# Optimization experiments

Measured on AMD Instinct MI355X. Metric: run time of the kernel, lower is better.

Reference implementation:

```python
import jax, jax.numpy as jnp
import numpy as np

HEADS = 4
DIM_HEAD = 32
IN_CHANNELS = 256
SCALE = DIM_HEAD ** -0.5
EPS = 1e-5


def setup_inputs() -> dict:
    key = jax.random.key(0)
    ks = jax.random.split(key, 6)
    B, C, H, W = 16, IN_CHANNELS, 64, 64
    inner = HEADS * DIM_HEAD  # 128
    x = jax.random.normal(ks[0], (B, C, H, W), dtype=jnp.float32)
    # 1x1 conv weights are [out_ch, in_ch] (kernel spatial dims are 1)
    w_qkv = jax.random.normal(ks[1], (3 * inner, C), dtype=jnp.float32) * (C ** -0.5)
    w_out = jax.random.normal(ks[2], (C, inner), dtype=jnp.float32) * (inner ** -0.5)
    b_out = jax.random.normal(ks[3], (C,), dtype=jnp.float32) * 0.01
    gn_gamma = jnp.ones((C,), dtype=jnp.float32)
    gn_beta = jnp.zeros((C,), dtype=jnp.float32)
    return {"x": x, "w_qkv": w_qkv, "w_out": w_out, "b_out": b_out,
            "gn_gamma": gn_gamma, "gn_beta": gn_beta}


def reference(x, w_qkv, w_out, b_out, gn_gamma, gn_beta):
    b, c, h, w = x.shape
    n = h * w
    inner = HEADS * DIM_HEAD
    # 1x1 conv (no bias): [b, 3*inner, h, w], then chunk into q,k,v along channels
    qkv = jnp.einsum('oc,bchw->bohw', w_qkv, x)
    qkv = qkv.reshape(b, 3, HEADS, DIM_HEAD, n)  # chunk + 'b (h c) x y -> b h c (x y)'
    q, k, v = qkv[:, 0], qkv[:, 1], qkv[:, 2]    # each [b, heads, dim_head, n]
    q = jax.nn.softmax(q, axis=-2) * SCALE       # softmax over dim_head axis
    k = jax.nn.softmax(k, axis=-1)               # softmax over spatial axis
    context = jnp.einsum('bhdn,bhen->bhde', k, v)  # [b, heads, d, e]
    out = jnp.einsum('bhde,bhdn->bhen', context, q)  # [b, heads, e, n]
    out = out.reshape(b, inner, h, w)            # 'b h c (x y) -> b (h c) x y'
    # out 1x1 conv with bias
    out = jnp.einsum('oc,bchw->bohw', w_out, out) + b_out[None, :, None, None]
    # GroupNorm(num_groups=1): normalize over (C,H,W) per sample, per-channel affine
    mean = jnp.mean(out, axis=(1, 2, 3), keepdims=True)
    var = jnp.var(out, axis=(1, 2, 3), keepdims=True)
    out = (out - mean) * jax.lax.rsqrt(var + EPS)
    return out * gn_gamma[None, :, None, None] + gn_beta[None, :, None, None]
```

## Files before the change

kernel.cpp:

```cpp
#include <hip/hip_runtime.h>
#include <hip/hip_bf16.h>
#include <math.h>

#define B_SZ 16
#define C_IN 256
#define HEADS 4
#define DHEAD 32
#define INNER 128
#define QKV_CH 384
#define N_PIX 4096
#define SCALE_Q 0.17677669529663687f
#define GN_EPS 1e-5f
#define NCHK 32

typedef __attribute__((ext_vector_type(8))) short s16x8;
typedef __attribute__((ext_vector_type(4))) float f32x4;
typedef __attribute__((ext_vector_type(8))) unsigned short u16x8;
typedef __attribute__((ext_vector_type(4))) unsigned short u16x4;

__device__ __forceinline__ float waveSum(float v) {
#pragma unroll
  for (int off = 32; off > 0; off >>= 1) v += __shfl_down(v, off, 64);
  return v;
}
__device__ __forceinline__ unsigned short f2bf(float f) {
  unsigned int u = __builtin_bit_cast(unsigned int, f);
  unsigned int r = 0x7FFFu + ((u >> 16) & 1u);
  return (unsigned short)((u + r) >> 16);
}
__device__ __forceinline__ float bf2f(unsigned short u) {
  unsigned int x = ((unsigned int)u) << 16;
  return __builtin_bit_cast(float, x);
}

__global__ __launch_bounds__(256) void cvt_w(const float* __restrict__ wq,
                                             const float* __restrict__ wo,
                                             unsigned short* __restrict__ wqb,
                                             unsigned short* __restrict__ wob) {
  const int i = blockIdx.x * 256 + threadIdx.x;
  if (i < QKV_CH * C_IN) wqb[i] = f2bf(wq[i]);
  if (i < C_IN * INNER) wob[i] = f2bf(wo[i]);
}

__global__ __launch_bounds__(512, 4) void qkv_gemm(const unsigned short* __restrict__ A,
                                                   const float* __restrict__ X,
                                                   unsigned short* __restrict__ Out) {
  const int b = blockIdx.y;
  const int n0 = blockIdx.x * 64;
  const int tid = threadIdx.x;
  const int w = tid >> 6, l = tid & 63;
  const int lr = l & 15, kg = l >> 4;
  const int wm = w >> 1, wn = w & 1;

  __shared__ char lds[65536];
  char* As = lds;
  char* Bs = lds + 49152;

  const float* xb = X + (size_t)b * C_IN * N_PIX;
  const int c_loc = ((tid >> 3) & 7) + w * 8;
  const int oct = tid & 7;

  auto ISSUE_A = [&](int kc, int half) {
#pragma unroll
    for (int it = 0; it < 3; ++it) {
      const int idx = it * 512 + tid;
      const int r = idx >> 3;
      const int srcb = ((idx & 7) << 4) ^ ((r & 7) << 4);
      __builtin_amdgcn_global_load_lds(
          (const __attribute__((address_space(1))) void*)((const char*)A +
              ((size_t)(half * 192 + r) * C_IN + kc * 64) * 2 + srcb),
          (__attribute__((address_space(3))) void*)(As + half * 24576 + idx * 16), 16, 0, 0);
    }
  };

  f32x4 xr0, xr1;
  auto ISSUE_X = [&](int kc) {
    const float* xp = xb + (size_t)(kc * 64 + c_loc) * N_PIX + n0 + oct * 8;
    xr0 = *reinterpret_cast<const f32x4*>(xp);
    xr1 = *reinterpret_cast<const f32x4*>(xp + 4);
  };

  auto WRITE_B = [&](int pb) {
#pragma unroll
    for (int j = 0; j < 8; ++j) {
      const int n = oct * 8 + j;
      const float v = (j < 4) ? xr0[j] : xr1[j - 4];
      *reinterpret_cast<unsigned short*>(
          Bs + pb * 8192 + n * 128 + ((2 * c_loc) ^ (((n ^ (n >> 3)) & 7) << 4))) = f2bf(v);
    }
  };

  f32x4 acc[2][3][2] = {};

  auto COMPUTE = [&](int kc, int half) {
    const char* Ab = As + half * 24576;
    const char* Bb = Bs + (kc & 1) * 8192;
#pragma unroll
    for (int ks = 0; ks < 2; ++ks) {
      const int kb = ks * 64 + kg * 16;
      s16x8 av[3], bv[2];
#pragma unroll
      for (int i = 0; i < 3; ++i) {
        const int r = wm * 48 + i * 16 + lr;
        av[i] = *reinterpret_cast<const s16x8*>(Ab + r * 128 + (kb ^ ((r & 7) << 4)));
      }
#pragma unroll
      for (int j = 0; j < 2; ++j) {
        const int n = wn * 32 + j * 16 + lr;
        bv[j] = *reinterpret_cast<const s16x8*>(Bb + n * 128 +
                                                (kb ^ (((n ^ (n >> 3)) & 7) << 4)));
      }
#pragma unroll
      for (int i = 0; i < 3; ++i)
#pragma unroll
        for (int j = 0; j < 2; ++j)
          acc[half][i][j] =
              __builtin_amdgcn_mfma_f32_16x16x32_bf16(av[i], bv[j], acc[half][i][j], 0, 0, 0);
    }
  };

  ISSUE_A(0, 0);
  ISSUE_X(0);
  asm volatile("s_waitcnt vmcnt(0)" ::: "memory");
  WRITE_B(0);
  asm volatile("s_waitcnt lgkmcnt(0)" ::: "memory");
  __builtin_amdgcn_s_barrier();

  for (int kc = 0; kc < 4; ++kc) {
    ISSUE_A(kc, 1);
    if (kc < 3) {
      ISSUE_X(kc + 1);
      asm volatile("s_waitcnt vmcnt(5)" ::: "memory");
    } else {
      asm volatile("s_waitcnt vmcnt(3)" ::: "memory");
    }
    __builtin_amdgcn_s_barrier();
    COMPUTE(kc, 0);
    asm volatile("s_waitcnt lgkmcnt(0)" ::: "memory");
    __builtin_amdgcn_s_barrier();
    if (kc < 3) {
      ISSUE_A(kc + 1, 0);
      asm volatile("s_waitcnt vmcnt(3)" ::: "memory");
    } else {
      asm volatile("s_waitcnt vmcnt(0)" ::: "memory");
    }
    __builtin_amdgcn_s_barrier();
    if (kc < 3) WRITE_B((kc + 1) & 1);
    COMPUTE(kc, 1);
    asm volatile("s_waitcnt lgkmcnt(0)" ::: "memory");
    __builtin_amdgcn_s_barrier();
  }

  unsigned short* Ob = Out + (size_t)b * QKV_CH * N_PIX;
#pragma unroll
  for (int half = 0; half < 2; ++half)
#pragma unroll
    for (int i = 0; i < 3; ++i) {
      const int mrow = half * 192 + wm * 48 + i * 16 + kg * 4;
#pragma unroll
      for (int j = 0; j < 2; ++j) {
        const int col = n0 + wn * 32 + j * 16 + lr;
#pragma unroll
        for (int r = 0; r < 4; ++r)
          Ob[(size_t)(mrow + r) * N_PIX + col] = f2bf(acc[half][i][j][r]);
      }
    }
}

__global__ __launch_bounds__(256) void ctx_mfma(const unsigned short* __restrict__ qkv,
                                                float* __restrict__ ctxp,
                                                float* __restrict__ mpart,
                                                float* __restrict__ spart) {
  const int wid = blockIdx.x * 4 + (threadIdx.x >> 6);
  const int l = threadIdx.x & 63;
  const int b = wid >> 7;
  const int h = (wid >> 5) & 3;
  const int c = wid & 31;
  const int lr = l & 15, kg = l >> 4;
  const unsigned short* kb =
      qkv + ((size_t)b * QKV_CH + INNER + h * DHEAD) * N_PIX + c * 128 + kg * 8;
  const unsigned short* vb = kb + (size_t)INNER * N_PIX;

  u16x8 kf[2][4], vf[2][4];
#pragma unroll
  for (int dt = 0; dt < 2; ++dt)
#pragma unroll
    for (int ks = 0; ks < 4; ++ks) {
      kf[dt][ks] = *reinterpret_cast<const u16x8*>(kb + (size_t)(dt * 16 + lr) * N_PIX + ks * 32);
      vf[dt][ks] = *reinterpret_cast<const u16x8*>(vb + (size_t)(dt * 16 + lr) * N_PIX + ks * 32);
    }
  float kv[2][4][8];
  float m[2] = {-INFINITY, -INFINITY};
#pragma unroll
  for (int dt = 0; dt < 2; ++dt)
#pragma unroll
    for (int ks = 0; ks < 4; ++ks)
#pragma unroll
      for (int j = 0; j < 8; ++j) {
        kv[dt][ks][j] = bf2f(kf[dt][ks][j]);
        m[dt] = fmaxf(m[dt], kv[dt][ks][j]);
      }
#pragma unroll
  for (int dt = 0; dt < 2; ++dt) {
    m[dt] = fmaxf(m[dt], __shfl_xor(m[dt], 16, 64));
    m[dt] = fmaxf(m[dt], __shfl_xor(m[dt], 32, 64));
  }
  float s[2] = {0.f, 0.f};
  s16x8 ka[2][4];
#pragma unroll
  for (int dt = 0; dt < 2; ++dt)
#pragma unroll
    for (int ks = 0; ks < 4; ++ks)
#pragma unroll
      for (int j = 0; j < 8; ++j) {
        const float e = __expf(kv[dt][ks][j] - m[dt]);
        s[dt] += e;
        ka[dt][ks][j] = (short)f2bf(e);
      }
#pragma unroll
  for (int dt = 0; dt < 2; ++dt) {
    s[dt] += __shfl_xor(s[dt], 16, 64);
    s[dt] += __shfl_xor(s[dt], 32, 64);
  }
  f32x4 acc[2][2] = {};
#pragma unroll
  for (int ks = 0; ks < 4; ++ks)
#pragma unroll
    for (int dt = 0; dt < 2; ++dt)
#pragma unroll
      for (int et = 0; et < 2; ++et)
        acc[dt][et] = __builtin_amdgcn_mfma_f32_16x16x32_bf16(
            ka[dt][ks], __builtin_bit_cast(s16x8, vf[et][ks]), acc[dt][et], 0, 0, 0);

  float* cp = ctxp + (size_t)wid * 1024;
#pragma unroll
  for (int dt = 0; dt < 2; ++dt)
#pragma unroll
    for (int et = 0; et < 2; ++et)
#pragma unroll
      for (int r = 0; r < 4; ++r)
        cp[(dt * 16 + kg * 4 + r) * 32 + et * 16 + lr] = acc[dt][et][r];
  if (kg == 0) {
    mpart[wid * 32 + lr] = m[0];
    mpart[wid * 32 + 16 + lr] = m[1];
    spart[wid * 32 + lr] = s[0];
    spart[wid * 32 + 16 + lr] = s[1];
  }
}

__global__ __launch_bounds__(256) void ctx_reduce(const float* __restrict__ ctxp,
                                                  const float* __restrict__ mpart,
                                                  const float* __restrict__ spart,
                                                  float* __restrict__ ctxf) {
  const int bh = blockIdx.x;
  const int tid = threadIdx.x;
  __shared__ float ms[NCHK][32], ss[NCHK][32], fac[NCHK][32];
  __shared__ float inv_l[32];
#pragma unroll
  for (int i = 0; i < 4; ++i) {
    const int idx = tid + i * 256;
    ms[idx >> 5][idx & 31] = mpart[(size_t)bh * 1024 + idx];
    ss[idx >> 5][idx & 31] = spart[(size_t)bh * 1024 + idx];
  }
  __syncthreads();
  if (tid < 32) {
    const int d = tid;
    float M = -INFINITY;
    for (int c = 0; c < NCHK; ++c) M = fmaxf(M, ms[c][d]);
    float den = 0.f;
    for (int c = 0; c < NCHK; ++c) {
      const float f = __expf(ms[c][d] - M);
      fac[c][d] = f;
      den += f * ss[c][d];
    }
    inv_l[d] = 1.0f / den;
  }
  __syncthreads();
  const float* cp = ctxp + (size_t)bh * (NCHK * 1024);
#pragma unroll
  for (int i = 0; i < 4; ++i) {
    const int idx = tid + i * 256;
    const int d = idx >> 5;
    float a = 0.f;
    for (int c = 0; c < NCHK; ++c) a += fac[c][d] * cp[(size_t)c * 1024 + idx];
    ctxf[(size_t)bh * 1024 + idx] = a * inv_l[d];
  }
}

__global__ __launch_bounds__(256) void weff_k(const unsigned short* __restrict__ wo,
                                              const float* __restrict__ ctxf,
                                              unsigned short* __restrict__ weff) {
  const int b = blockIdx.z, h = blockIdx.y, oq = blockIdx.x;
  const int tid = threadIdx.x;
  const int o = oq * 64 + (tid >> 2);
  const int d0 = (tid & 3) * 8;

  float wr[32];
  const unsigned short* wp = wo + (size_t)o * INNER + h * DHEAD;
#pragma unroll
  for (int e8 = 0; e8 < 4; ++e8) {
    u16x8 v = *reinterpret_cast<const u16x8*>(wp + e8 * 8);
#pragma unroll
    for (int j = 0; j < 8; ++j) wr[e8 * 8 + j] = bf2f(v[j]);
  }
  const float* cb = ctxf + (size_t)(b * HEADS + h) * 1024;
  u16x8 outv;
#pragma unroll
  for (int dd = 0; dd < 8; ++dd) {
    const float* cr = cb + (size_t)(d0 + dd) * 32;
    float acc = 0.f;
#pragma unroll
    for (int e4 = 0; e4 < 8; ++e4) {
      const f32x4 c4 = *reinterpret_cast<const f32x4*>(cr + e4 * 4);
#pragma unroll
      for (int j = 0; j < 4; ++j) acc += wr[e4 * 4 + j] * c4[j];
    }
    outv[dd] = f2bf(acc);
  }
  unsigned short* op = weff + ((size_t)b * C_IN + o) * INNER + h * DHEAD + d0;
  *reinterpret_cast<u16x8*>(op) = outv;
}

__global__ __launch_bounds__(256) void q_softmax(const unsigned short* __restrict__ qkv,
                                                 unsigned short* __restrict__ qsm_t) {
  const int b = blockIdx.z, h = blockIdx.y;
  const int n = blockIdx.x * 256 + threadIdx.x;
  const unsigned short* qb = qkv + ((size_t)b * QKV_CH + h * DHEAD) * N_PIX + n;
  float q[32];
  float m = -INFINITY;
#pragma unroll
  for (int d2 = 0; d2 < 32; ++d2) {
    q[d2] = bf2f(qb[(size_t)d2 * N_PIX]);
    m = fmaxf(m, q[d2]);
  }
  float s = 0.f;
#pragma unroll
  for (int d2 = 0; d2 < 32; ++d2) {
    q[d2] = __expf(q[d2] - m);
    s += q[d2];
  }
  const float inv = SCALE_Q / s;
  unsigned short* ob = qsm_t + ((size_t)b * N_PIX + n) * INNER + h * DHEAD;
#pragma unroll
  for (int d8 = 0; d8 < 4; ++d8) {
    u16x8 pk;
#pragma unroll
    for (int r = 0; r < 8; ++r) pk[r] = f2bf(q[d8 * 8 + r] * inv);
    *reinterpret_cast<u16x8*>(&ob[d8 * 8]) = pk;
  }
}

template <bool WRITE>
__global__ __launch_bounds__(256) void out_gemm_t(
    const unsigned short* __restrict__ A, const unsigned short* __restrict__ Bm,
    float* __restrict__ Out, const float* __restrict__ bias,
    float* __restrict__ gn_part, const float* __restrict__ gamma,
    const float* __restrict__ beta) {
  const int b = blockIdx.z;
  const int m0 = blockIdx.y * 128;
  const int n0 = blockIdx.x * 128;
  const int tid = threadIdx.x;
  const int w = tid >> 6, l = tid & 63;
  const int lr = l & 15, kg = l >> 4;
  const int mOff = (w >> 1) * 64, nOff = (w & 1) * 64;

  __shared__ unsigned short As[8192];
  __shared__ unsigned short Bs[8192];
  __shared__ float red[8];

  const unsigned short* Ab = A + (size_t)b * C_IN * INNER;
  const unsigned short* Bb = Bm + (size_t)b * N_PIX * INNER;
  f32x4 acc[4][4] = {};

  for (int kc = 0; kc < INNER; kc += 64) {
#pragma unroll
    for (int s = 0; s < 4; ++s) {
      const int blk = (w * 4 + s) * 64 + l;
      const int r = blk >> 3;
      const int c = ((blk & 7) ^ (r & 7)) << 3;
      __builtin_amdgcn_global_load_lds(
          (const __attribute__((address_space(1))) void*)(Ab + (size_t)(m0 + r) * INNER + kc + c),
          (__attribute__((address_space(3))) void*)((char*)As + (w * 4 + s) * 1024), 16, 0, 0);
      __builtin_amdgcn_global_load_lds(
          (const __attribute__((address_space(1))) void*)(Bb + (size_t)(n0 + r) * INNER + kc + c),
          (__attribute__((address_space(3))) void*)((char*)Bs + (w * 4 + s) * 1024), 16, 0, 0);
    }
    __syncthreads();
#pragma unroll
    for (int ks = 0; ks < 2; ++ks) {
      const int kbyte = ks * 64 + kg * 16;
      s16x8 av[4], bv[4];
#pragma unroll
      for (int i = 0; i < 4; ++i) {
        const int row = mOff + i * 16 + lr;
        av[i] = *reinterpret_cast<const s16x8*>(
            (const char*)As + row * 128 + (kbyte ^ ((row & 7) << 4)));
      }
#pragma unroll
      for (int j = 0; j < 4; ++j) {
        const int row = nOff + j * 16 + lr;
        bv[j] = *reinterpret_cast<const s16x8*>(
            (const char*)Bs + row * 128 + (kbyte ^ ((row & 7) << 4)));
      }
#pragma unroll
      for (int i = 0; i < 4; ++i)
#pragma unroll
        for (int j = 0; j < 4; ++j)
          acc[i][j] = __builtin_amdgcn_mfma_f32_16x16x32_bf16(av[i], bv[j], acc[i][j], 0, 0, 0);
    }
    __syncthreads();
  }

  if (!WRITE) {
    float s = 0.f, s2 = 0.f;
#pragma unroll
    for (int i = 0; i < 4; ++i) {
      const int rowb = m0 + mOff + i * 16 + kg * 4;
#pragma unroll
      for (int r = 0; r < 4; ++r) {
        const float bvs = bias[rowb + r];
#pragma unroll
        for (int j = 0; j < 4; ++j) {
          const float v = acc[i][j][r] + bvs;
          s += v;
          s2 += v * v;
        }
      }
    }
    const float S = waveSum(s), S2 = waveSum(s2);
    if (l == 0) {
      red[w] = S;
      red[4 + w] = S2;
    }
    __syncthreads();
    if (tid == 0) {
      const int bid = (b * 2 + blockIdx.y) * 32 + blockIdx.x;
      gn_part[(size_t)bid * 2 + 0] = red[0] + red[1] + red[2] + red[3];
      gn_part[(size_t)bid * 2 + 1] = red[4] + red[5] + red[6] + red[7];
    }
  } else {
    const int i64 = tid & 63;
    float ps = gn_part[(size_t)(b * 64 + i64) * 2 + 0];
    float ps2 = gn_part[(size_t)(b * 64 + i64) * 2 + 1];
    ps = waveSum(ps);
    ps2 = waveSum(ps2);
    const float invn = 1.0f / (float)(C_IN * N_PIX);
    const float mean = __shfl(ps, 0, 64) * invn;
    const float var = __shfl(ps2, 0, 64) * invn - mean * mean;
    const float istd = rsqrtf(var + GN_EPS);

    float* Ob = Out + (size_t)b * C_IN * N_PIX;
#pragma unroll
    for (int i = 0; i < 4; ++i) {
      const int rowb = m0 + mOff + i * 16 + kg * 4;
#pragma unroll
      for (int r = 0; r < 4; ++r) {
        const int ch = rowb + r;
        const float bvs = bias[ch];
        const float g = gamma[ch] * istd;
        const float be = beta[ch];
#pragma unroll
        for (int j = 0; j < 4; ++j) {
          const int col = n0 + nOff + j * 16 + lr;
          const float v = acc[i][j][r] + bvs;
          Ob[(size_t)ch * N_PIX + col] = (v - mean) * g + be;
        }
      }
    }
  }
}

extern "C" void kernel_launch(void* const* d_in, const int* in_sizes, int n_in,
                              void* d_out, int out_size, void* d_ws, size_t ws_size,
                              hipStream_t stream) {
  const float* x = (const float*)d_in[0];
  const float* w_qkv = (const float*)d_in[1];
  const float* w_out = (const float*)d_in[2];
  const float* b_out = (const float*)d_in[3];
  const float* gamma = (const float*)d_in[4];
  const float* beta = (const float*)d_in[5];
  float* out = (float*)d_out;

  char* p = (char*)d_ws;
  unsigned short* qkv_bf = (unsigned short*)p; p += (size_t)B_SZ * QKV_CH * N_PIX * 2;
  unsigned short* qsm_t = (unsigned short*)p;  p += (size_t)B_SZ * N_PIX * INNER * 2;
  unsigned short* wq_bf = (unsigned short*)p;  p += (size_t)QKV_CH * C_IN * 2;
  unsigned short* wo_bf = (unsigned short*)p;  p += (size_t)C_IN * INNER * 2;
  float* ctxp = (float*)p;    p += (size_t)B_SZ * HEADS * NCHK * 1024 * 4;
  float* mpart = (float*)p;   p += (size_t)B_SZ * HEADS * NCHK * 32 * 4;
  float* spart = (float*)p;   p += (size_t)B_SZ * HEADS * NCHK * 32 * 4;
  float* ctxf = (float*)p;    p += (size_t)B_SZ * HEADS * 1024 * 4;
  unsigned short* weff = (unsigned short*)p; p += (size_t)B_SZ * C_IN * INNER * 2;
  float* gn_part = (float*)p; p += (size_t)1024 * 2 * 4;

  cvt_w<<<dim3(384), 256, 0, stream>>>(w_qkv, w_out, wq_bf, wo_bf);
  qkv_gemm<<<dim3(64, B_SZ), 512, 0, stream>>>(wq_bf, x, qkv_bf);
  ctx_mfma<<<dim3(512), 256, 0, stream>>>(qkv_bf, ctxp, mpart, spart);
  ctx_reduce<<<dim3(64), 256, 0, stream>>>(ctxp, mpart, spart, ctxf);
  weff_k<<<dim3(4, HEADS, B_SZ), 256, 0, stream>>>(wo_bf, ctxf, weff);
  q_softmax<<<dim3(16, HEADS, B_SZ), 256, 0, stream>>>(qkv_bf, qsm_t);
  out_gemm_t<false><<<dim3(32, 2, B_SZ), 256, 0, stream>>>(
      weff, qsm_t, nullptr, b_out, gn_part, nullptr, nullptr);
  out_gemm_t<true><<<dim3(32, 2, B_SZ), 256, 0, stream>>>(
      weff, qsm_t, out, b_out, gn_part, gamma, beta);
}
```

Measured before the change: 98.91 us.

## Swizzle block order for XCD locality and deepen qkv GEMM load pipeline

Flattens grids and remaps block IDs so consecutive ranks on each of the 8 XCDs cover contiguous batch/pixel ranges. This is meant to improve L2 locality in qkv_gemm, ctx_mfma, q_softmax and out_gemm. qkv_gemm is rewritten as a fully unrolled pipeline: each wave loads only its own A rows, X is double-registered (XA/XB) and prefetched two stages ahead, and vmcnt waits are relaxed with fewer barriers. The risks are more registers per thread and fragile hand-tuned waitcnt ordering.

```diff
diff --git a/kernel.cpp b/kernel.cpp
--- a/kernel.cpp
+++ b/kernel.cpp
@@ -18,6 +18,10 @@
 typedef __attribute__((ext_vector_type(8))) unsigned short u16x8;
 typedef __attribute__((ext_vector_type(4))) unsigned short u16x4;
 
+#define VMCNT(n) asm volatile("s_waitcnt vmcnt(" #n ")" ::: "memory")
+#define LGKMCNT0 asm volatile("s_waitcnt lgkmcnt(0)" ::: "memory")
+#define CFENCE asm volatile("" ::: "memory")
+
 __device__ __forceinline__ float waveSum(float v) {
 #pragma unroll
   for (int off = 32; off > 0; off >>= 1) v += __shfl_down(v, off, 64);
@@ -45,8 +49,10 @@
 __global__ __launch_bounds__(512, 4) void qkv_gemm(const unsigned short* __restrict__ A,
                                                    const float* __restrict__ X,
                                                    unsigned short* __restrict__ Out) {
-  const int b = blockIdx.y;
-  const int n0 = blockIdx.x * 64;
+  const int id = blockIdx.x;
+  const int rank = (id & 7) * 128 + (id >> 3);
+  const int b = rank >> 6;
+  const int n0 = (rank & 63) * 64;
   const int tid = threadIdx.x;
   const int w = tid >> 6, l = tid & 63;
   const int lr = l & 15, kg = l >> 4;
@@ -56,35 +62,49 @@
   char* As = lds;
   char* Bs = lds + 49152;
 
-  const float* xb = X + (size_t)b * C_IN * N_PIX;
   const int c_loc = ((tid >> 3) & 7) + w * 8;
   const int oct = tid & 7;
+  const float* xbase = X + (size_t)b * C_IN * N_PIX + (size_t)c_loc * N_PIX + n0 + oct * 8;
 
   auto ISSUE_A = [&](int kc, int half) {
 #pragma unroll
-    for (int it = 0; it < 3; ++it) {
-      const int idx = it * 512 + tid;
-      const int r = idx >> 3;
-      const int srcb = ((idx & 7) << 4) ^ ((r & 7) << 4);
+    for (int it = 0; it < 6; ++it) {
+      const int idx = it * 64 + l;
+      const int row = wm * 48 + (idx >> 3);
+      const int srcb = ((idx & 7) << 4) ^ ((row & 7) << 4);
       __builtin_amdgcn_global_load_lds(
           (const __attribute__((address_space(1))) void*)((const char*)A +
-              ((size_t)(half * 192 + r) * C_IN + kc * 64) * 2 + srcb),
-          (__attribute__((address_space(3))) void*)(As + half * 24576 + idx * 16), 16, 0, 0);
+              ((size_t)(half * 192 + row) * C_IN + kc * 64) * 2 + srcb),
+          (__attribute__((address_space(3))) void*)(As + half * 24576 + wm * 6144 + idx * 16),
+          16, 0, 0);
     }
   };
 
-  f32x4 xr0, xr1;
-  auto ISSUE_X = [&](int kc) {
-    const float* xp = xb + (size_t)(kc * 64 + c_loc) * N_PIX + n0 + oct * 8;
-    xr0 = *reinterpret_cast<const f32x4*>(xp);
-    xr1 = *reinterpret_cast<const f32x4*>(xp + 4);
+  f32x4 xa0, xa1, xb0, xb1;
+  auto ISSUE_XA = [&](int kc) {
+    const float* xp = xbase + (size_t)(kc * 64) * N_PIX;
+    xa0 = *reinterpret_cast<const f32x4*>(xp);
+    xa1 = *reinterpret_cast<const f32x4*>(xp + 4);
   };
-
-  auto WRITE_B = [&](int pb) {
+  auto ISSUE_XB = [&](int kc) {
+    const float* xp = xbase + (size_t)(kc * 64) * N_PIX;
+    xb0 = *reinterpret_cast<const f32x4*>(xp);
+    xb1 = *reinterpret_cast<const f32x4*>(xp + 4);
+  };
+  auto WRITE_BA = [&](int pb) {
 #pragma unroll
     for (int j = 0; j < 8; ++j) {
       const int n = oct * 8 + j;
-      const float v = (j < 4) ? xr0[j] : xr1[j - 4];
+      const float v = (j < 4) ? xa0[j] : xa1[j - 4];
+      *reinterpret_cast<unsigned short*>(
+          Bs + pb * 8192 + n * 128 + ((2 * c_loc) ^ (((n ^ (n >> 3)) & 7) << 4))) = f2bf(v);
+    }
+  };
+  auto WRITE_BB = [&](int pb) {
+#pragma unroll
+    for (int j = 0; j < 8; ++j) {
+      const int n = oct * 8 + j;
+      const float v = (j < 4) ? xb0[j] : xb1[j - 4];
       *reinterpret_cast<unsigned short*>(
           Bs + pb * 8192 + n * 128 + ((2 * c_loc) ^ (((n ^ (n >> 3)) & 7) << 4))) = f2bf(v);
     }
@@ -119,37 +139,53 @@
     }
   };
 
-  ISSUE_A(0, 0);
-  ISSUE_X(0);
-  asm volatile("s_waitcnt vmcnt(0)" ::: "memory");
-  WRITE_B(0);
-  asm volatile("s_waitcnt lgkmcnt(0)" ::: "memory");
-  __builtin_amdgcn_s_barrier();
-
-  for (int kc = 0; kc < 4; ++kc) {
-    ISSUE_A(kc, 1);
-    if (kc < 3) {
-      ISSUE_X(kc + 1);
-      asm volatile("s_waitcnt vmcnt(5)" ::: "memory");
-    } else {
-      asm volatile("s_waitcnt vmcnt(3)" ::: "memory");
-    }
-    __builtin_amdgcn_s_barrier();
-    COMPUTE(kc, 0);
-    asm volatile("s_waitcnt lgkmcnt(0)" ::: "memory");
-    __builtin_amdgcn_s_barrier();
-    if (kc < 3) {
-      ISSUE_A(kc + 1, 0);
-      asm volatile("s_waitcnt vmcnt(3)" ::: "memory");
-    } else {
-      asm volatile("s_waitcnt vmcnt(0)" ::: "memory");
-    }
-    __builtin_amdgcn_s_barrier();
-    if (kc < 3) WRITE_B((kc + 1) & 1);
-    COMPUTE(kc, 1);
-    asm volatile("s_waitcnt lgkmcnt(0)" ::: "memory");
-    __builtin_amdgcn_s_barrier();
-  }
+  ISSUE_A(0, 0); CFENCE;
+  ISSUE_XA(0);
+  VMCNT(0);
+  WRITE_BA(0);
+  LGKMCNT0;
+  __builtin_amdgcn_s_barrier();
+
+  ISSUE_A(0, 1); CFENCE;
+  ISSUE_XB(1);
+  COMPUTE(0, 0);
+  LGKMCNT0;
+  __builtin_amdgcn_s_barrier();
+  ISSUE_A(1, 0); CFENCE;
+  ISSUE_XA(2);
+  VMCNT(8);
+  WRITE_BB(1);
+  COMPUTE(0, 1);
+  LGKMCNT0;
+  __builtin_amdgcn_s_barrier();
+  ISSUE_A(1, 1);
+  VMCNT(8);
+  COMPUTE(1, 0);
+  LGKMCNT0;
+  __builtin_amdgcn_s_barrier();
+  ISSUE_A(2, 0); CFENCE;
+  ISSUE_XB(3);
+  VMCNT(8);
+  WRITE_BA(0);
+  COMPUTE(1, 1);
+  LGKMCNT0;
+  __builtin_amdgcn_s_barrier();
+  ISSUE_A(2, 1);
+  VMCNT(8);
+  COMPUTE(2, 0);
+  LGKMCNT0;
+  __builtin_amdgcn_s_barrier();
+  ISSUE_A(3, 0);
+  VMCNT(6);
+  WRITE_BB(1);
+  COMPUTE(2, 1);
+  LGKMCNT0;
+  __builtin_amdgcn_s_barrier();
+  ISSUE_A(3, 1);
+  VMCNT(6);
+  COMPUTE(3, 0);
+  VMCNT(0);
+  COMPUTE(3, 1);
 
   unsigned short* Ob = Out + (size_t)b * QKV_CH * N_PIX;
 #pragma unroll
@@ -171,7 +207,9 @@
                                                 float* __restrict__ ctxp,
                                                 float* __restrict__ mpart,
                                                 float* __restrict__ spart) {
-  const int wid = blockIdx.x * 4 + (threadIdx.x >> 6);
+  const int id = blockIdx.x;
+  const int rank = (id & 7) * 64 + (id >> 3);
+  const int wid = rank * 4 + (threadIdx.x >> 6);
   const int l = threadIdx.x & 63;
   const int b = wid >> 7;
   const int h = (wid >> 5) & 3;
@@ -323,8 +361,11 @@
 
 __global__ __launch_bounds__(256) void q_softmax(const unsigned short* __restrict__ qkv,
                                                  unsigned short* __restrict__ qsm_t) {
-  const int b = blockIdx.z, h = blockIdx.y;
-  const int n = blockIdx.x * 256 + threadIdx.x;
+  const int id = blockIdx.x;
+  const int rank = (id & 7) * 128 + (id >> 3);
+  const int b = rank >> 6;
+  const int h = (rank >> 4) & 3;
+  const int n = (rank & 15) * 256 + threadIdx.x;
   const unsigned short* qb = qkv + ((size_t)b * QKV_CH + h * DHEAD) * N_PIX + n;
   float q[32];
   float m = -INFINITY;
@@ -356,9 +397,11 @@
     float* __restrict__ Out, const float* __restrict__ bias,
     float* __restrict__ gn_part, const float* __restrict__ gamma,
     const float* __restrict__ beta) {
-  const int b = blockIdx.z;
-  const int m0 = blockIdx.y * 128;
-  const int n0 = blockIdx.x * 128;
+  const int id = blockIdx.x;
+  const int rank = (id & 7) * 128 + (id >> 3);
+  const int b = rank >> 6;
+  const int m0 = ((rank >> 5) & 1) * 128;
+  const int n0 = (rank & 31) * 128;
   const int tid = threadIdx.x;
   const int w = tid >> 6, l = tid & 63;
   const int lr = l & 15, kg = l >> 4;
@@ -434,9 +477,8 @@
     }
     __syncthreads();
     if (tid == 0) {
-      const int bid = (b * 2 + blockIdx.y) * 32 + blockIdx.x;
-      gn_part[(size_t)bid * 2 + 0] = red[0] + red[1] + red[2] + red[3];
-      gn_part[(size_t)bid * 2 + 1] = red[4] + red[5] + red[6] + red[7];
+      gn_part[(size_t)rank * 2 + 0] = red[0] + red[1] + red[2] + red[3];
+      gn_part[(size_t)rank * 2 + 1] = red[4] + red[5] + red[6] + red[7];
     }
   } else {
     const int i64 = tid & 63;
@@ -494,13 +536,13 @@
   float* gn_part = (float*)p; p += (size_t)1024 * 2 * 4;
 
   cvt_w<<<dim3(384), 256, 0, stream>>>(w_qkv, w_out, wq_bf, wo_bf);
-  qkv_gemm<<<dim3(64, B_SZ), 512, 0, stream>>>(wq_bf, x, qkv_bf);
+  qkv_gemm<<<dim3(1024), 512, 0, stream>>>(wq_bf, x, qkv_bf);
   ctx_mfma<<<dim3(512), 256, 0, stream>>>(qkv_bf, ctxp, mpart, spart);
   ctx_reduce<<<dim3(64), 256, 0, stream>>>(ctxp, mpart, spart, ctxf);
   weff_k<<<dim3(4, HEADS, B_SZ), 256, 0, stream>>>(wo_bf, ctxf, weff);
-  q_softmax<<<dim3(16, HEADS, B_SZ), 256, 0, stream>>>(qkv_bf, qsm_t);
-  out_gemm_t<false><<<dim3(32, 2, B_SZ), 256, 0, stream>>>(
+  q_softmax<<<dim3(1024), 256, 0, stream>>>(qkv_bf, qsm_t);
+  out_gemm_t<false><<<dim3(1024), 256, 0, stream>>>(
       weff, qsm_t, nullptr, b_out, gn_part, nullptr, nullptr);
-  out_gemm_t<true><<<dim3(32, 2, B_SZ), 256, 0, stream>>>(
+  out_gemm_t<true><<<dim3(1024), 256, 0, stream>>>(
       weff, qsm_t, out, b_out, gn_part, gamma, beta);
 }
```

Result: slower. 101.4 us (+2.5%).

## Fuse query softmax into QKV GEMM epilogue and remap blocks for XCD locality

Applied to the files above, without the earlier changes.

The q-channel softmax over the head dimension now runs inside the QKV GEMM epilogue: q accumulators are staged in LDS, softmaxed per pixel and head, and written transposed as bf16. The q channels are no longer stored to the intermediate qkv buffer, and the separate q_softmax kernel is removed. This removes a kernel launch and a full re-read of q from global memory. Separately, the qkv_gemm, ctx_mfma and out_gemm kernels use a 1D grid with a rank permutation ((id&7)*K + id>>3) so that neighbouring tiles land on the same XCD for L2 reuse. In exchange the GEMM epilogue gains an LDS pass and an extra barrier.

```diff
diff --git a/kernel.cpp b/kernel.cpp
--- a/kernel.cpp
+++ b/kernel.cpp
@@ -18,6 +18,9 @@
 typedef __attribute__((ext_vector_type(8))) unsigned short u16x8;
 typedef __attribute__((ext_vector_type(4))) unsigned short u16x4;
 
+#define VMCNT(n) asm volatile("s_waitcnt vmcnt(" #n ")" ::: "memory")
+#define LGKMCNT0 asm volatile("s_waitcnt lgkmcnt(0)" ::: "memory")
+
 __device__ __forceinline__ float waveSum(float v) {
 #pragma unroll
   for (int off = 32; off > 0; off >>= 1) v += __shfl_down(v, off, 64);
@@ -44,9 +47,12 @@
 
 __global__ __launch_bounds__(512, 4) void qkv_gemm(const unsigned short* __restrict__ A,
                                                    const float* __restrict__ X,
-                                                   unsigned short* __restrict__ Out) {
-  const int b = blockIdx.y;
-  const int n0 = blockIdx.x * 64;
+                                                   unsigned short* __restrict__ Out,
+                                                   unsigned short* __restrict__ qsm_t) {
+  const int id = blockIdx.x;
+  const int rank = (id & 7) * 128 + (id >> 3);
+  const int b = rank >> 6;
+  const int n0 = (rank & 63) * 64;
   const int tid = threadIdx.x;
   const int w = tid >> 6, l = tid & 63;
   const int lr = l & 15, kg = l >> 4;
@@ -56,9 +62,9 @@
   char* As = lds;
   char* Bs = lds + 49152;
 
-  const float* xb = X + (size_t)b * C_IN * N_PIX;
   const int c_loc = ((tid >> 3) & 7) + w * 8;
   const int oct = tid & 7;
+  const float* xbase = X + (size_t)b * C_IN * N_PIX + (size_t)c_loc * N_PIX + n0 + oct * 8;
 
   auto ISSUE_A = [&](int kc, int half) {
 #pragma unroll
@@ -75,7 +81,7 @@
 
   f32x4 xr0, xr1;
   auto ISSUE_X = [&](int kc) {
-    const float* xp = xb + (size_t)(kc * 64 + c_loc) * N_PIX + n0 + oct * 8;
+    const float* xp = xbase + (size_t)(kc * 64) * N_PIX;
     xr0 = *reinterpret_cast<const f32x4*>(xp);
     xr1 = *reinterpret_cast<const f32x4*>(xp + 4);
   };
@@ -121,33 +127,33 @@
 
   ISSUE_A(0, 0);
   ISSUE_X(0);
-  asm volatile("s_waitcnt vmcnt(0)" ::: "memory");
+  VMCNT(0);
   WRITE_B(0);
-  asm volatile("s_waitcnt lgkmcnt(0)" ::: "memory");
+  LGKMCNT0;
   __builtin_amdgcn_s_barrier();
 
   for (int kc = 0; kc < 4; ++kc) {
     ISSUE_A(kc, 1);
     if (kc < 3) {
       ISSUE_X(kc + 1);
-      asm volatile("s_waitcnt vmcnt(5)" ::: "memory");
+      VMCNT(5);
     } else {
-      asm volatile("s_waitcnt vmcnt(3)" ::: "memory");
+      VMCNT(3);
     }
     __builtin_amdgcn_s_barrier();
     COMPUTE(kc, 0);
-    asm volatile("s_waitcnt lgkmcnt(0)" ::: "memory");
+    LGKMCNT0;
     __builtin_amdgcn_s_barrier();
     if (kc < 3) {
       ISSUE_A(kc + 1, 0);
-      asm volatile("s_waitcnt vmcnt(3)" ::: "memory");
+      VMCNT(3);
     } else {
-      asm volatile("s_waitcnt vmcnt(0)" ::: "memory");
+      VMCNT(0);
     }
     __builtin_amdgcn_s_barrier();
     if (kc < 3) WRITE_B((kc + 1) & 1);
     COMPUTE(kc, 1);
-    asm volatile("s_waitcnt lgkmcnt(0)" ::: "memory");
+    LGKMCNT0;
     __builtin_amdgcn_s_barrier();
   }
 
@@ -156,22 +162,74 @@
   for (int half = 0; half < 2; ++half)
 #pragma unroll
     for (int i = 0; i < 3; ++i) {
-      const int mrow = half * 192 + wm * 48 + i * 16 + kg * 4;
+      const int mt = wm * 48 + i * 16;
+      if (half == 1 || mt >= 128) {
+        const int mrow = half * 192 + mt + kg * 4;
+#pragma unroll
+        for (int j = 0; j < 2; ++j) {
+          const int col = n0 + wn * 32 + j * 16 + lr;
+#pragma unroll
+          for (int r = 0; r < 4; ++r)
+            Ob[(size_t)(mrow + r) * N_PIX + col] = f2bf(acc[half][i][j][r]);
+        }
+      }
+    }
+
+  float* qs = (float*)lds;
+#pragma unroll
+  for (int i = 0; i < 3; ++i) {
+    const int mt = wm * 48 + i * 16;
+    if (mt < 128) {
+      const int rowb = mt + kg * 4;
 #pragma unroll
       for (int j = 0; j < 2; ++j) {
-        const int col = n0 + wn * 32 + j * 16 + lr;
-#pragma unroll
-        for (int r = 0; r < 4; ++r)
-          Ob[(size_t)(mrow + r) * N_PIX + col] = f2bf(acc[half][i][j][r]);
-      }
-    }
+        const int c_l = wn * 32 + j * 16 + lr;
+        *reinterpret_cast<f32x4*>(qs + c_l * 132 + rowb) = acc[0][i][j];
+      }
+    }
+  }
+  LGKMCNT0;
+  __builtin_amdgcn_s_barrier();
+
+  if (tid < 256) {
+    const int n_loc = tid & 63, h = tid >> 6;
+    const float* qrow = qs + n_loc * 132 + h * 32;
+    f32x4 qv[8];
+#pragma unroll
+    for (int c = 0; c < 8; ++c) qv[c] = *reinterpret_cast<const f32x4*>(qrow + c * 4);
+    float m = qv[0][0];
+#pragma unroll
+    for (int c = 0; c < 8; ++c)
+#pragma unroll
+      for (int r = 0; r < 4; ++r) m = fmaxf(m, qv[c][r]);
+    float e[32];
+    float s = 0.f;
+#pragma unroll
+    for (int c = 0; c < 8; ++c)
+#pragma unroll
+      for (int r = 0; r < 4; ++r) {
+        e[c * 4 + r] = __expf(qv[c][r] - m);
+        s += e[c * 4 + r];
+      }
+    const float inv = SCALE_Q / s;
+    unsigned short* ob = qsm_t + ((size_t)b * N_PIX + n0 + n_loc) * INNER + h * DHEAD;
+#pragma unroll
+    for (int d8 = 0; d8 < 4; ++d8) {
+      u16x8 pk;
+#pragma unroll
+      for (int r = 0; r < 8; ++r) pk[r] = f2bf(e[d8 * 8 + r] * inv);
+      *reinterpret_cast<u16x8*>(&ob[d8 * 8]) = pk;
+    }
+  }
 }
 
 __global__ __launch_bounds__(256) void ctx_mfma(const unsigned short* __restrict__ qkv,
                                                 float* __restrict__ ctxp,
                                                 float* __restrict__ mpart,
                                                 float* __restrict__ spart) {
-  const int wid = blockIdx.x * 4 + (threadIdx.x >> 6);
+  const int id = blockIdx.x;
+  const int rank = (id & 7) * 64 + (id >> 3);
+  const int wid = rank * 4 + (threadIdx.x >> 6);
   const int l = threadIdx.x & 63;
   const int b = wid >> 7;
   const int h = (wid >> 5) & 3;
@@ -321,44 +379,17 @@
   *reinterpret_cast<u16x8*>(op) = outv;
 }
 
-__global__ __launch_bounds__(256) void q_softmax(const unsigned short* __restrict__ qkv,
-                                                 unsigned short* __restrict__ qsm_t) {
-  const int b = blockIdx.z, h = blockIdx.y;
-  const int n = blockIdx.x * 256 + threadIdx.x;
-  const unsigned short* qb = qkv + ((size_t)b * QKV_CH + h * DHEAD) * N_PIX + n;
-  float q[32];
-  float m = -INFINITY;
-#pragma unroll
-  for (int d2 = 0; d2 < 32; ++d2) {
-    q[d2] = bf2f(qb[(size_t)d2 * N_PIX]);
-    m = fmaxf(m, q[d2]);
-  }
-  float s = 0.f;
-#pragma unroll
-  for (int d2 = 0; d2 < 32; ++d2) {
-    q[d2] = __expf(q[d2] - m);
-    s += q[d2];
-  }
-  const float inv = SCALE_Q / s;
-  unsigned short* ob = qsm_t + ((size_t)b * N_PIX + n) * INNER + h * DHEAD;
-#pragma unroll
-  for (int d8 = 0; d8 < 4; ++d8) {
-    u16x8 pk;
-#pragma unroll
-    for (int r = 0; r < 8; ++r) pk[r] = f2bf(q[d8 * 8 + r] * inv);
-    *reinterpret_cast<u16x8*>(&ob[d8 * 8]) = pk;
-  }
-}
-
 template <bool WRITE>
 __global__ __launch_bounds__(256) void out_gemm_t(
     const unsigned short* __restrict__ A, const unsigned short* __restrict__ Bm,
     float* __restrict__ Out, const float* __restrict__ bias,
     float* __restrict__ gn_part, const float* __restrict__ gamma,
     const float* __restrict__ beta) {
-  const int b = blockIdx.z;
-  const int m0 = blockIdx.y * 128;
-  const int n0 = blockIdx.x * 128;
+  const int id = blockIdx.x;
+  const int rank = (id & 7) * 128 + (id >> 3);
+  const int b = rank >> 6;
+  const int m0 = ((rank >> 5) & 1) * 128;
+  const int n0 = (rank & 31) * 128;
   const int tid = threadIdx.x;
   const int w = tid >> 6, l = tid & 63;
   const int lr = l & 15, kg = l >> 4;
@@ -434,9 +465,8 @@
     }
     __syncthreads();
     if (tid == 0) {
-      const int bid = (b * 2 + blockIdx.y) * 32 + blockIdx.x;
-      gn_part[(size_t)bid * 2 + 0] = red[0] + red[1] + red[2] + red[3];
-      gn_part[(size_t)bid * 2 + 1] = red[4] + red[5] + red[6] + red[7];
+      gn_part[(size_t)rank * 2 + 0] = red[0] + red[1] + red[2] + red[3];
+      gn_part[(size_t)rank * 2 + 1] = red[4] + red[5] + red[6] + red[7];
     }
   } else {
     const int i64 = tid & 63;
@@ -494,13 +524,12 @@
   float* gn_part = (float*)p; p += (size_t)1024 * 2 * 4;
 
   cvt_w<<<dim3(384), 256, 0, stream>>>(w_qkv, w_out, wq_bf, wo_bf);
-  qkv_gemm<<<dim3(64, B_SZ), 512, 0, stream>>>(wq_bf, x, qkv_bf);
+  qkv_gemm<<<dim3(1024), 512, 0, stream>>>(wq_bf, x, qkv_bf, qsm_t);
   ctx_mfma<<<dim3(512), 256, 0, stream>>>(qkv_bf, ctxp, mpart, spart);
   ctx_reduce<<<dim3(64), 256, 0, stream>>>(ctxp, mpart, spart, ctxf);
   weff_k<<<dim3(4, HEADS, B_SZ), 256, 0, stream>>>(wo_bf, ctxf, weff);
-  q_softmax<<<dim3(16, HEADS, B_SZ), 256, 0, stream>>>(qkv_bf, qsm_t);
-  out_gemm_t<false><<<dim3(32, 2, B_SZ), 256, 0, stream>>>(
+  out_gemm_t<false><<<dim3(1024), 256, 0, stream>>>(
       weff, qsm_t, nullptr, b_out, gn_part, nullptr, nullptr);
-  out_gemm_t<true><<<dim3(32, 2, B_SZ), 256, 0, stream>>>(
+  out_gemm_t<true><<<dim3(1024), 256, 0, stream>>>(
       weff, qsm_t, out, b_out, gn_part, gamma, beta);
 }
```

New measurement: 92.75 us. 1.07x faster.
